# Kernel tuning notes

Hardware: AMD Instinct MI355X
Metric: run time of the kernel (lower is better)

## Reference

```python
import jax, jax.numpy as jnp
import numpy as np

B, V = 128, 128000
N_GREEDY = 8  # rows with temperature == 0 to exercise the argmax fallback


def setup_inputs() -> dict:
    key = jax.random.key(0)
    k1, k2, k3, k4 = jax.random.split(key, 4)
    logits = jax.random.normal(k1, (B, V), dtype=jnp.float32)
    temperatures = jax.random.uniform(k2, (B, 1), dtype=jnp.float32, minval=0.1, maxval=1.5)
    temperatures = temperatures.at[:N_GREEDY].set(0.0)  # greedy rows
    top_ps = 0.5 + 0.5 * jax.random.uniform(k3, (B, 1), dtype=jnp.float32)  # in [0.5, 1.0]
    top_ks = jax.random.randint(k4, (B, 1), 1, 64).astype(jnp.float32)  # stored as float, like torch code
    return {"logits": logits, "temperatures": temperatures, "top_ps": top_ps, "top_ks": top_ks}


def reference(logits, temperatures, top_ps, top_ks):
    # Temperature scale (temp==0 rows use safe temperature 1.0, overridden by greedy below)
    safe_t = jnp.where(temperatures == 0.0, 1.0, temperatures)  # [B,1]
    scaled = logits / safe_t  # [B,V] -- this is the `probs` returned by the torch module

    probs = jax.nn.softmax(scaled, axis=-1)  # [B,V]

    # Descending sort over vocab
    order = jnp.argsort(-probs, axis=-1)                      # [B,V] int
    sorted_probs = jnp.take_along_axis(probs, order, axis=-1)  # [B,V]
    cum = jnp.cumsum(sorted_probs, axis=-1)                    # [B,V]

    ranks = jnp.arange(V, dtype=jnp.float32)[None, :]          # [1,V]
    keep_k = ranks < top_ks                                    # top-k mask  [B,V]
    keep_p = (cum - sorted_probs) < top_ps                     # top-p mask (cumprob before token < p)
    keep = (keep_k & keep_p) | (ranks == 0.0)                  # always keep the top-1 token

    # Joint filter + Gumbel-max sampling (equivalent to renormalize-then-categorical)
    logp = jnp.where(keep, jnp.log(sorted_probs), -jnp.inf)    # [B,V]
    g = jax.random.gumbel(jax.random.key(42), (B, V), dtype=jnp.float32)
    sampled_sorted = jnp.argmax(logp + g, axis=-1)             # [B] index in sorted space
    sampled = jnp.take_along_axis(order, sampled_sorted[:, None], axis=-1)[:, 0]  # back to vocab ids

    # Greedy fallback for temperature == 0 rows (argmax of ORIGINAL logits)
    greedy = jnp.argmax(logits, axis=-1)
    ids = jnp.where(temperatures[:, 0] == 0.0, greedy, sampled).astype(jnp.int32)

    return ids, scaled
```

## Files before the change

### kernel.cpp

```cpp
#include <hip/hip_runtime.h>
#include <stdint.h>

#define NB 128
#define NV 128000
#define TOPC 63

#define JPB 25
#define CH 5120
#define CH4 1280
#define K1T 256
#define QPT 5
#define HB 8192
#define HBW (HB / 2)
#define CSLOT 104
#define SCCAP (JPB * CSLOT)
#define NHB 2048
#define SNCAP 256
#define NBLK1 (NB * JPB)

#define WS_CS_OFF   0
#define WS_CS_BYTES ((size_t)NBLK1 * CSLOT * 4)
#define WS_M_OFF    (WS_CS_BYTES)
#define WS_S_OFF    (WS_M_OFF + NBLK1 * 4)
#define WS_CNT_OFF  (WS_S_OFF + NBLK1 * 4)
#define WS_CTR_OFF  (WS_CNT_OFF + NBLK1 * 4)
#define WS_CI_OFF   (WS_CTR_OFF + NB * 4)
#define WS_NEED     (WS_CI_OFF + (size_t)NBLK1 * CSLOT * 2)

#define NT 1024
#define NV4 (NV / 4)
#define NBINS 16384
#define CCAP 2048

typedef float f4 __attribute__((ext_vector_type(4)));

__device__ __forceinline__ uint32_t rotl32(uint32_t v, uint32_t d) {
  return (v << d) | (v >> (32u - d));
}

__device__ __forceinline__ void threefry2x32(uint32_t k0, uint32_t k1,
                                             uint32_t x0, uint32_t x1,
                                             uint32_t& o0, uint32_t& o1) {
  uint32_t ks2 = k0 ^ k1 ^ 0x1BD11BDAu;
  x0 += k0; x1 += k1;
#define TF_ROUND(r) { x0 += x1; x1 = rotl32(x1, (r)); x1 ^= x0; }
  TF_ROUND(13) TF_ROUND(15) TF_ROUND(26) TF_ROUND(6)
  x0 += k1;  x1 += ks2 + 1u;
  TF_ROUND(17) TF_ROUND(29) TF_ROUND(16) TF_ROUND(24)
  x0 += ks2; x1 += k0 + 2u;
  TF_ROUND(13) TF_ROUND(15) TF_ROUND(26) TF_ROUND(6)
  x0 += k0;  x1 += k1 + 3u;
  TF_ROUND(17) TF_ROUND(29) TF_ROUND(16) TF_ROUND(24)
  x0 += k1;  x1 += ks2 + 4u;
  TF_ROUND(13) TF_ROUND(15) TF_ROUND(26) TF_ROUND(6)
  x0 += ks2; x1 += k0 + 5u;
#undef TF_ROUND
  o0 = x0; o1 = x1;
}

__device__ __forceinline__ uint32_t jax_random_bits_u32(uint64_t n) {
  uint32_t o0, o1;
  threefry2x32(0u, 42u, (uint32_t)(n >> 32), (uint32_t)n, o0, o1);
  return o0 ^ o1;
}

__device__ __forceinline__ float gumbel_from_bits(uint32_t bits) {
  const float tiny = 1.17549435e-38f;
  float f = __uint_as_float(0x3f800000u | (bits >> 9)) - 1.0f;
  float u = f * 1.0f + tiny;
  u = fmaxf(tiny, u);
  return -logf(-logf(u));
}

__device__ __forceinline__ uint32_t sortkey(float x) {
  uint32_t b = __float_as_uint(x);
  uint32_t mask = (uint32_t)((int32_t)b >> 31) | 0x80000000u;
  return b ^ mask;
}

__device__ __forceinline__ float div_exact(float a, float st, float ry) {
  float q0 = a * ry;
  float r  = __builtin_fmaf(-st, q0, a);
  return __builtin_fmaf(r, ry, q0);
}

__global__ __launch_bounds__(K1T) void k1_scan(
    const float* __restrict__ logits, const float* __restrict__ temps,
    float* __restrict__ out, uint32_t* __restrict__ cand_s,
    uint16_t* __restrict__ cand_i, float* __restrict__ m_arr,
    float* __restrict__ S_arr, uint32_t* __restrict__ cnt_arr) {

  __shared__ uint32_t histw[HBW];
  __shared__ uint32_t ssum[K1T];
  __shared__ float swm[4], sws[4];
  __shared__ uint32_t swc[4];
  __shared__ int s_tstar;
  __shared__ uint32_t s_cutkey, s_lcnt;

  const int bid = blockIdx.x;
  const int r = bid / JPB, j = bid - r * JPB;
  const int t = threadIdx.x;
  const int lane = t & 63, wv = t >> 6;
  const float temp = temps[r];
  const float st = (temp == 0.0f) ? 1.0f : temp;
  const float ry = 1.0f / st;

  const f4* __restrict__ lrow4 = (const f4*)(logits + (size_t)r * NV + (size_t)j * CH);
  f4* __restrict__ srow4 = (f4*)(out + NB + (size_t)r * NV + (size_t)j * CH);

  for (int i = t; i < HBW; i += K1T) histw[i] = 0u;
  if (t == 0) { s_tstar = K1T - 1; s_lcnt = 0u; }
  __syncthreads();

  f4 sreg[QPT];
  float mx0 = -INFINITY, mx1 = -INFINITY, mx2 = -INFINITY, mx3 = -INFINITY;
  float sm0 = 0.0f, sm1 = 0.0f, sm2 = 0.0f, sm3 = 0.0f;
  #pragma unroll
  for (int q = 0; q < QPT; ++q) {
    int i = q * K1T + t;
    f4 x = lrow4[i];
    f4 s;
    s.x = div_exact(x.x, st, ry);
    s.y = div_exact(x.y, st, ry);
    s.z = div_exact(x.z, st, ry);
    s.w = div_exact(x.w, st, ry);
    srow4[i] = s;
    sreg[q] = s;
    mx0 = fmaxf(mx0, s.x); mx1 = fmaxf(mx1, s.y);
    mx2 = fmaxf(mx2, s.z); mx3 = fmaxf(mx3, s.w);
    sm0 += __expf(s.x); sm1 += __expf(s.y);
    sm2 += __expf(s.z); sm3 += __expf(s.w);
  }
  float mx = fmaxf(fmaxf(mx0, mx1), fmaxf(mx2, mx3));
  float sum = (sm0 + sm1) + (sm2 + sm3);
  #pragma unroll
  for (int off = 32; off > 0; off >>= 1) {
    mx = fmaxf(mx, __shfl_xor(mx, off));
    sum += __shfl_xor(sum, off);
  }
  if (lane == 0) { swm[wv] = mx; sws[wv] = sum; }
  __syncthreads();
  const float mxb = fmaxf(fmaxf(swm[0], swm[1]), fmaxf(swm[2], swm[3]));
  if (t == 0) {
    m_arr[bid] = mxb;
    S_arr[bid] = sws[0] + sws[1] + sws[2] + sws[3];
  }
  const float thr = mxb - 3.0f * ry;

  uint32_t myc = 0;
  #pragma unroll
  for (int q = 0; q < QPT; ++q) {
    float sv[4] = {sreg[q].x, sreg[q].y, sreg[q].z, sreg[q].w};
    #pragma unroll
    for (int c = 0; c < 4; ++c) {
      if (sv[c] >= thr) {
        uint32_t b = sortkey(sv[c]) >> 19;
        atomicAdd(&histw[b >> 1], (b & 1) ? 65536u : 1u);
        ++myc;
      }
    }
  }
  #pragma unroll
  for (int off = 32; off > 0; off >>= 1) myc += __shfl_xor(myc, off);
  if (lane == 0) swc[wv] = myc;
  __syncthreads();
  const uint32_t tot = swc[0] + swc[1] + swc[2] + swc[3];
  if (tot < 63u) {
    for (int i = t; i < HBW; i += K1T) histw[i] = 0u;
    __syncthreads();
    #pragma unroll
    for (int q = 0; q < QPT; ++q) {
      float sv[4] = {sreg[q].x, sreg[q].y, sreg[q].z, sreg[q].w};
      #pragma unroll
      for (int c = 0; c < 4; ++c) {
        uint32_t b = sortkey(sv[c]) >> 19;
        atomicAdd(&histw[b >> 1], (b & 1) ? 65536u : 1u);
      }
    }
    __syncthreads();
  }

  uint32_t sloc = 0;
  #pragma unroll
  for (int u = 0; u < 16; ++u) {
    uint32_t w = histw[t * 16 + u];
    sloc += (w & 0xFFFFu) + (w >> 16);
  }
  ssum[t] = sloc;
  __syncthreads();
  for (int off = 1; off < K1T; off <<= 1) {
    uint32_t v = ssum[t] + ((t + off < K1T) ? ssum[t + off] : 0u);
    __syncthreads();
    ssum[t] = v;
    __syncthreads();
  }
  if (ssum[t] >= 63u && (t == K1T - 1 || ssum[t + 1] < 63u)) s_tstar = t;
  __syncthreads();
  if (t == 0) {
    int ts = s_tstar;
    uint32_t running = (ts == K1T - 1) ? 0u : ssum[ts + 1];
    int cutbin = ts * 32;
    for (int q = 31; q >= 0; --q) {
      uint32_t w = histw[ts * 16 + (q >> 1)];
      uint32_t c = (q & 1) ? (w >> 16) : (w & 0xFFFFu);
      running += c;
      if (running >= 63u) { cutbin = ts * 32 + q; break; }
    }
    s_cutkey = (uint32_t)cutbin << 19;
  }
  __syncthreads();
  const uint32_t cutkey = s_cutkey;

  uint32_t* __restrict__ mys = cand_s + (size_t)bid * CSLOT;
  uint16_t* __restrict__ myi = cand_i + (size_t)bid * CSLOT;
  #pragma unroll
  for (int q = 0; q < QPT; ++q) {
    float sv[4] = {sreg[q].x, sreg[q].y, sreg[q].z, sreg[q].w};
    #pragma unroll
    for (int c = 0; c < 4; ++c) {
      if (sortkey(sv[c]) >= cutkey) {
        uint32_t pos = atomicAdd(&s_lcnt, 1u);
        if (pos < CSLOT) {
          mys[pos] = __float_as_uint(sv[c]);
          myi[pos] = (uint16_t)((q * K1T + t) * 4 + c);
        }
      }
    }
  }
  __syncthreads();
  if (t == 0) cnt_arr[bid] = (s_lcnt < CSLOT) ? s_lcnt : (uint32_t)CSLOT;
}

__global__ __launch_bounds__(K1T) void k2_final(
    const float* __restrict__ temps, const float* __restrict__ topps,
    const float* __restrict__ topks, const uint32_t* __restrict__ cand_s,
    const uint16_t* __restrict__ cand_i, const float* __restrict__ m_arr,
    const float* __restrict__ S_arr, const uint32_t* __restrict__ cnt_arr,
    float* __restrict__ out) {

  __shared__ unsigned long long sc[SCCAP];
  __shared__ uint32_t nhist[NHB];
  __shared__ unsigned long long sn[SNCAP];
  __shared__ float sm8[32], ss8[32];
  __shared__ uint32_t scnt8[JPB];
  __shared__ uint32_t swsum[4];
  __shared__ uint32_t s_cutp, s_scnt;
  __shared__ uint32_t soff[JPB + 1];
  __shared__ float s_m, s_Z;
  __shared__ float sp[TOPC], scum[TOPC], slv[TOPC];
  __shared__ int sidx_[TOPC];

  const int r = blockIdx.x;
  const int t = threadIdx.x;
  const int lane = t & 63, wv = t >> 6;
  const float temp = temps[r];

  if (t < 32) {
    sm8[t] = (t < JPB) ? m_arr[r * JPB + t] : -INFINITY;
    ss8[t] = (t < JPB) ? S_arr[r * JPB + t] : 0.0f;
  }
  if (t < JPB) scnt8[t] = cnt_arr[r * JPB + t];
  for (int i = t; i < NHB; i += K1T) nhist[i] = 0u;
  __syncthreads();
  if (t == 0) {
    float m = -INFINITY;
    for (int q = 0; q < JPB; ++q) m = fmaxf(m, sm8[q]);
    float Sr = 0.0f;
    for (int q = 0; q < JPB; ++q) Sr += ss8[q];
    s_m = m;
    s_Z = Sr * expf(-m);
    uint32_t off = 0;
    for (int q = 0; q < JPB; ++q) { soff[q] = off; off += scnt8[q]; }
    soff[JPB] = off;
    s_scnt = 0u;
  }
  __syncthreads();
  const float m = s_m, Z = s_Z;
  const int total = (int)soff[JPB];

  for (int e = t; e < total; e += K1T) {
    int q = 0;
    while (e >= (int)soff[q + 1]) ++q;
    int slot = (r * JPB + q) * CSLOT + (e - (int)soff[q]);
    float s = __uint_as_float(cand_s[slot]);
    uint32_t idx = (uint32_t)q * CH + (uint32_t)cand_i[slot];
    float p = expf(s - m) / Z;
    unsigned long long v = ((unsigned long long)__float_as_uint(p) << 32)
                         | (unsigned long long)(0xFFFFFFFFu - idx);
    sc[e] = v;
    atomicAdd(&nhist[__float_as_uint(p) >> 21], 1u);
  }
  __syncthreads();

  uint32_t nloc = 0;
  #pragma unroll
  for (int u = 0; u < 8; ++u) nloc += nhist[t * 8 + u];
  uint32_t ns = nloc;
  #pragma unroll
  for (int off = 1; off < 64; off <<= 1) {
    uint32_t v = __shfl_down(ns, off);
    if (lane + off < 64) ns += v;
  }
  if (lane == 0) swsum[wv] = ns;
  __syncthreads();
  #pragma unroll
  for (int w2 = 0; w2 < 4; ++w2)
    if (w2 > wv) ns += swsum[w2];
  if (ns >= 63u && (ns - nloc) < 63u) {
    uint32_t running = ns - nloc;
    int cutbin = t * 8;
    for (int u = 7; u >= 0; --u) {
      running += nhist[t * 8 + u];
      if (running >= 63u) { cutbin = t * 8 + u; break; }
    }
    s_cutp = (uint32_t)cutbin << 21;
  }
  __syncthreads();
  const uint32_t cutp = s_cutp;

  for (int e = t; e < total; e += K1T) {
    unsigned long long v = sc[e];
    if ((uint32_t)(v >> 32) >= cutp) {
      uint32_t pos = atomicAdd(&s_scnt, 1u);
      if (pos < SNCAP) sn[pos] = v;
    }
  }
  __syncthreads();
  const uint32_t scnt = s_scnt;
  if (t < SNCAP && t >= (int)scnt) sn[t] = 0ull;
  __syncthreads();

  for (int k = 2; k <= SNCAP; k <<= 1) {
    for (int jj = k >> 1; jj > 0; jj >>= 1) {
      int e = t;
      int ixj = e ^ jj;
      if (ixj > e) {
        unsigned long long a = sn[e], c = sn[ixj];
        bool desc = ((e & k) == 0);
        if (desc ? (a < c) : (a > c)) { sn[e] = c; sn[ixj] = a; }
      }
      __syncthreads();
    }
  }

  if (t < TOPC) {
    unsigned long long kv = sn[t];
    sp[t] = __uint_as_float((uint32_t)(kv >> 32));
    sidx_[t] = (int)(0xFFFFFFFFu - (uint32_t)(kv & 0xFFFFFFFFull));
  }
  __syncthreads();
  if (t == 0) {
    float L0[63], L1[31], L2[15], L3[7], L4[3];
    for (int i = 0; i < 63; ++i) L0[i] = sp[i];
    for (int i = 0; i < 31; ++i) L1[i] = L0[2*i] + L0[2*i+1];
    for (int i = 0; i < 15; ++i) L2[i] = L1[2*i] + L1[2*i+1];
    for (int i = 0; i < 7;  ++i) L3[i] = L2[2*i] + L2[2*i+1];
    for (int i = 0; i < 3;  ++i) L4[i] = L3[2*i] + L3[2*i+1];
    float S5 = L4[0] + L4[1];
    float S4[3]; S4[0] = L4[0]; S4[1] = S5; S4[2] = S5 + L4[2];
    float S3[7]; S3[0] = L3[0];
    for (int k = 0; k < 3; ++k) { S3[2*k+1] = S4[k]; if (2*k+2 < 7)  S3[2*k+2] = S4[k] + L3[2*k+2]; }
    float S2[15]; S2[0] = L2[0];
    for (int k = 0; k < 7; ++k) { S2[2*k+1] = S3[k]; if (2*k+2 < 15) S2[2*k+2] = S3[k] + L2[2*k+2]; }
    float S1[31]; S1[0] = L1[0];
    for (int k = 0; k < 15; ++k){ S1[2*k+1] = S2[k]; if (2*k+2 < 31) S1[2*k+2] = S2[k] + L1[2*k+2]; }
    scum[0] = L0[0];
    for (int k = 0; k < 31; ++k){ scum[2*k+1] = S1[k]; if (2*k+2 < 63) scum[2*k+2] = S1[k] + L0[2*k+2]; }
  }
  __syncthreads();
  if (t < TOPC) {
    const float topp = topps[r];
    const float topk = topks[r];
    bool keep = (((float)t < topk) && ((scum[t] - sp[t]) < topp)) || (t == 0);
    uint32_t bits = jax_random_bits_u32((uint64_t)r * NV + (uint64_t)t);
    float g = gumbel_from_bits(bits);
    slv[t] = keep ? (logf(sp[t]) + g) : -INFINITY;
  }
  __syncthreads();
  if (t == 0) {
    float best = slv[0]; int br = 0;
    for (int q = 1; q < TOPC; ++q)
      if (slv[q] > best) { best = slv[q]; br = q; }
    int id = (temp == 0.0f) ? sidx_[0] : sidx_[br];
    out[r] = (float)id;
  }
}


__global__ __launch_bounds__(NT) void sampler_kernel(
    const float* __restrict__ logits, const float* __restrict__ temps,
    const float* __restrict__ topps, const float* __restrict__ topks,
    float* __restrict__ out) {

  __shared__ union {
    uint32_t hist[NBINS];
    unsigned long long cand[CCAP];
  } sh;
  __shared__ uint32_t ssum[NT];
  __shared__ float redf[NT];
  __shared__ uint32_t s_cutkey, s_cnt;
  __shared__ int s_tstar;
  __shared__ float sp[TOPC], scum[TOPC], slv[TOPC];
  __shared__ int sidx_[TOPC];

  const int b = blockIdx.x;
  const int t = threadIdx.x;
  const float temp = temps[b];
  const float st = (temp == 0.0f) ? 1.0f : temp;
  const float topp = topps[b];
  const float topk = topks[b];

  const float4* __restrict__ lrow = (const float4*)(logits + (size_t)b * NV);
  float4* __restrict__ srow = (float4*)(out + NB + (size_t)b * NV);

  for (int i = t; i < NBINS; i += NT) sh.hist[i] = 0u;
  if (t == 0) s_tstar = NT - 1;

  float lmax = -INFINITY;
  for (int i = t; i < NV4; i += NT) {
    float4 x = lrow[i];
    float4 s;
    s.x = x.x / st; s.y = x.y / st; s.z = x.z / st; s.w = x.w / st;
    srow[i] = s;
    lmax = fmaxf(lmax, fmaxf(fmaxf(s.x, s.y), fmaxf(s.z, s.w)));
  }
  redf[t] = lmax;
  __syncthreads();
  for (int off = NT / 2; off > 0; off >>= 1) {
    if (t < off) redf[t] = fmaxf(redf[t], redf[t + off]);
    __syncthreads();
  }
  const float m = redf[0];
  __syncthreads();

  float lsum = 0.0f;
  for (int i = t; i < NV4; i += NT) {
    float4 x = lrow[i];
    float s0 = x.x / st, s1 = x.y / st, s2 = x.z / st, s3 = x.w / st;
    lsum += expf(s0 - m); lsum += expf(s1 - m);
    lsum += expf(s2 - m); lsum += expf(s3 - m);
    atomicAdd(&sh.hist[sortkey(s0) >> 18], 1u);
    atomicAdd(&sh.hist[sortkey(s1) >> 18], 1u);
    atomicAdd(&sh.hist[sortkey(s2) >> 18], 1u);
    atomicAdd(&sh.hist[sortkey(s3) >> 18], 1u);
  }
  redf[t] = lsum;
  __syncthreads();
  for (int off = NT / 2; off > 0; off >>= 1) {
    if (t < off) redf[t] += redf[t + off];
    __syncthreads();
  }
  const float Z = redf[0];
  __syncthreads();

  uint32_t sloc = 0;
  #pragma unroll
  for (int j = 0; j < 16; ++j) sloc += sh.hist[t * 16 + j];
  ssum[t] = sloc;
  __syncthreads();
  for (int off = 1; off < NT; off <<= 1) {
    uint32_t v = ssum[t] + ((t + off < NT) ? ssum[t + off] : 0u);
    __syncthreads();
    ssum[t] = v;
    __syncthreads();
  }
  if (ssum[t] >= 63u && (t == NT - 1 || ssum[t + 1] < 63u)) s_tstar = t;
  __syncthreads();
  if (t == 0) {
    int ts = s_tstar;
    uint32_t running = (ts == NT - 1) ? 0u : ssum[ts + 1];
    int cutbin = ts * 16;
    for (int j = 15; j >= 0; --j) {
      running += sh.hist[ts * 16 + j];
      if (running >= 63u) { cutbin = ts * 16 + j; break; }
    }
    s_cutkey = (uint32_t)cutbin << 18;
    s_cnt = 0u;
  }
  __syncthreads();
  const uint32_t cutkey = s_cutkey;

  for (int i = t; i < NV4; i += NT) {
    float4 x = lrow[i];
    float sv[4];
    sv[0] = x.x / st; sv[1] = x.y / st; sv[2] = x.z / st; sv[3] = x.w / st;
    #pragma unroll
    for (int j = 0; j < 4; ++j) {
      uint32_t key = sortkey(sv[j]);
      if (key >= cutkey) {
        float p = expf(sv[j] - m) / Z;
        uint32_t pos = atomicAdd(&s_cnt, 1u);
        if (pos < CCAP) {
          uint32_t idx = (uint32_t)(i * 4 + j);
          sh.cand[pos] = ((unsigned long long)__float_as_uint(p) << 32)
                       | (unsigned long long)(0xFFFFFFFFu - idx);
        }
      }
    }
  }
  __syncthreads();
  const uint32_t cnt = s_cnt;
  for (int e = t; e < CCAP; e += NT)
    if ((uint32_t)e >= cnt) sh.cand[e] = 0ull;
  __syncthreads();

  for (uint32_t k = 2; k <= CCAP; k <<= 1) {
    for (uint32_t j = k >> 1; j > 0; j >>= 1) {
      for (int e = t; e < CCAP; e += NT) {
        uint32_t ixj = (uint32_t)e ^ j;
        if (ixj > (uint32_t)e) {
          unsigned long long a = sh.cand[e], c = sh.cand[ixj];
          bool desc = (((uint32_t)e & k) == 0u);
          if (desc ? (a < c) : (a > c)) { sh.cand[e] = c; sh.cand[ixj] = a; }
        }
      }
      __syncthreads();
    }
  }

  if (t < TOPC) {
    unsigned long long kv = sh.cand[t];
    sp[t] = __uint_as_float((uint32_t)(kv >> 32));
    sidx_[t] = (int)(0xFFFFFFFFu - (uint32_t)(kv & 0xFFFFFFFFull));
  }
  __syncthreads();
  if (t == 0) {
    float L0[63], L1[31], L2[15], L3[7], L4[3];
    for (int i = 0; i < 63; ++i) L0[i] = sp[i];
    for (int i = 0; i < 31; ++i) L1[i] = L0[2*i] + L0[2*i+1];
    for (int i = 0; i < 15; ++i) L2[i] = L1[2*i] + L1[2*i+1];
    for (int i = 0; i < 7;  ++i) L3[i] = L2[2*i] + L2[2*i+1];
    for (int i = 0; i < 3;  ++i) L4[i] = L3[2*i] + L3[2*i+1];
    float S5 = L4[0] + L4[1];
    float S4[3]; S4[0] = L4[0]; S4[1] = S5; S4[2] = S5 + L4[2];
    float S3[7]; S3[0] = L3[0];
    for (int k = 0; k < 3; ++k) { S3[2*k+1] = S4[k]; if (2*k+2 < 7)  S3[2*k+2] = S4[k] + L3[2*k+2]; }
    float S2[15]; S2[0] = L2[0];
    for (int k = 0; k < 7; ++k) { S2[2*k+1] = S3[k]; if (2*k+2 < 15) S2[2*k+2] = S3[k] + L2[2*k+2]; }
    float S1[31]; S1[0] = L1[0];
    for (int k = 0; k < 15; ++k){ S1[2*k+1] = S2[k]; if (2*k+2 < 31) S1[2*k+2] = S2[k] + L1[2*k+2]; }
    scum[0] = L0[0];
    for (int k = 0; k < 31; ++k){ scum[2*k+1] = S1[k]; if (2*k+2 < 63) scum[2*k+2] = S1[k] + L0[2*k+2]; }
  }
  __syncthreads();
  if (t < TOPC) {
    bool keep = (((float)t < topk) && ((scum[t] - sp[t]) < topp)) || (t == 0);
    uint32_t bits = jax_random_bits_u32((uint64_t)b * NV + (uint64_t)t);
    float g = gumbel_from_bits(bits);
    slv[t] = keep ? (logf(sp[t]) + g) : -INFINITY;
  }
  __syncthreads();
  if (t == 0) {
    float best = slv[0]; int br = 0;
    for (int q = 1; q < TOPC; ++q)
      if (slv[q] > best) { best = slv[q]; br = q; }
    int id = (temp == 0.0f) ? sidx_[0] : sidx_[br];
    out[b] = (float)id;
  }
}

extern "C" void kernel_launch(void* const* d_in, const int* in_sizes, int n_in,
                              void* d_out, int out_size, void* d_ws, size_t ws_size,
                              hipStream_t stream) {
  const float* logits = (const float*)d_in[0];
  const float* temps  = (const float*)d_in[1];
  const float* topps  = (const float*)d_in[2];
  const float* topks  = (const float*)d_in[3];
  float* out = (float*)d_out;

  if (ws_size >= WS_NEED) {
    uint32_t* cand_s  = (uint32_t*)((char*)d_ws + WS_CS_OFF);
    uint16_t* cand_i  = (uint16_t*)((char*)d_ws + WS_CI_OFF);
    float*    m_arr   = (float*)((char*)d_ws + WS_M_OFF);
    float*    S_arr   = (float*)((char*)d_ws + WS_S_OFF);
    uint32_t* cnt_arr = (uint32_t*)((char*)d_ws + WS_CNT_OFF);
    hipLaunchKernelGGL(k1_scan, dim3(NBLK1), dim3(K1T), 0, stream,
                       logits, temps, out, cand_s, cand_i, m_arr, S_arr, cnt_arr);
    hipLaunchKernelGGL(k2_final, dim3(NB), dim3(K1T), 0, stream,
                       temps, topps, topks, cand_s, cand_i,
                       m_arr, S_arr, cnt_arr, out);
  } else {
    hipLaunchKernelGGL(sampler_kernel, dim3(NB), dim3(NT), 0, stream,
                       logits, temps, topps, topks, out);
  }
}
```

Baseline: 51.76 us.

## Use max-relative linear histogram for candidate cutoff with radix fallback

In the scan kernel, a single 256-bin histogram over the scaled distance from the block max (a window of about 2.2 raw-logit units) replaces the thresholded radix-key histogram. A wave-shuffle prefix scan over those bins finds the cut, and candidates are written directly. The old 8192-bin radix path runs only when the count falls outside [63, CSLOT]. The final kernel drops the serial prefix-offset computation and iterates over fixed per-block slots, masking by count. This trades some wasted iterations over empty slots for less serial work.

```diff
diff --git a/kernel.cpp b/kernel.cpp
--- a/kernel.cpp
+++ b/kernel.cpp
@@ -12,6 +12,7 @@
 #define QPT 5
 #define HB 8192
 #define HBW (HB / 2)
+#define WINSD 2.2f
 #define CSLOT 104
 #define SCCAP (JPB * CSLOT)
 #define NHB 2048
@@ -93,9 +94,9 @@
   __shared__ uint32_t histw[HBW];
   __shared__ uint32_t ssum[K1T];
   __shared__ float swm[4], sws[4];
-  __shared__ uint32_t swc[4];
+  __shared__ uint32_t wtot[4];
   __shared__ int s_tstar;
-  __shared__ uint32_t s_cutkey, s_lcnt;
+  __shared__ uint32_t s_cutbin, s_cutkey, s_lcnt;
 
   const int bid = blockIdx.x;
   const int r = bid / JPB, j = bid - r * JPB;
@@ -108,9 +109,8 @@
   const f4* __restrict__ lrow4 = (const f4*)(logits + (size_t)r * NV + (size_t)j * CH);
   f4* __restrict__ srow4 = (f4*)(out + NB + (size_t)r * NV + (size_t)j * CH);
 
-  for (int i = t; i < HBW; i += K1T) histw[i] = 0u;
-  if (t == 0) { s_tstar = K1T - 1; s_lcnt = 0u; }
-  __syncthreads();
+  histw[t] = 0u;
+  if (t == 0) { s_lcnt = 0u; s_tstar = K1T - 1; s_cutbin = 255u; }
 
   f4 sreg[QPT];
   float mx0 = -INFINITY, mx1 = -INFINITY, mx2 = -INFINITY, mx3 = -INFINITY;
@@ -145,41 +145,76 @@
     m_arr[bid] = mxb;
     S_arr[bid] = sws[0] + sws[1] + sws[2] + sws[3];
   }
-  const float thr = mxb - 3.0f * ry;
-
-  uint32_t myc = 0;
+  const float F = (256.0f / WINSD) * st;
+
   #pragma unroll
   for (int q = 0; q < QPT; ++q) {
     float sv[4] = {sreg[q].x, sreg[q].y, sreg[q].z, sreg[q].w};
     #pragma unroll
     for (int c = 0; c < 4; ++c) {
-      if (sv[c] >= thr) {
-        uint32_t b = sortkey(sv[c]) >> 19;
-        atomicAdd(&histw[b >> 1], (b & 1) ? 65536u : 1u);
-        ++myc;
+      float d = (mxb - sv[c]) * F;
+      if (d < 256.0f) atomicAdd(&histw[(uint32_t)d], 1u);
+    }
+  }
+  __syncthreads();
+
+  {
+    uint32_t c = histw[t];
+    uint32_t ps = c;
+    #pragma unroll
+    for (int off = 1; off < 64; off <<= 1) {
+      uint32_t v = __shfl_up(ps, off);
+      if (lane >= off) ps += v;
+    }
+    if (lane == 63) wtot[wv] = ps;
+    __syncthreads();
+    uint32_t add = 0;
+    #pragma unroll
+    for (int w2 = 0; w2 < 4; ++w2)
+      if (w2 < wv) add += wtot[w2];
+    ps += add;
+    if (ps >= 63u && (ps - c) < 63u) s_cutbin = (uint32_t)t;
+  }
+  __syncthreads();
+  const uint32_t cutbin = s_cutbin;
+
+  uint32_t* __restrict__ mys = cand_s + (size_t)bid * CSLOT;
+  uint16_t* __restrict__ myi = cand_i + (size_t)bid * CSLOT;
+  #pragma unroll
+  for (int q = 0; q < QPT; ++q) {
+    float sv[4] = {sreg[q].x, sreg[q].y, sreg[q].z, sreg[q].w};
+    #pragma unroll
+    for (int c = 0; c < 4; ++c) {
+      float d = (mxb - sv[c]) * F;
+      if (d < 256.0f && (uint32_t)d <= cutbin) {
+        uint32_t pos = atomicAdd(&s_lcnt, 1u);
+        if (pos < CSLOT) {
+          mys[pos] = __float_as_uint(sv[c]);
+          myi[pos] = (uint16_t)((q * K1T + t) * 4 + c);
+        }
       }
     }
   }
-  #pragma unroll
-  for (int off = 32; off > 0; off >>= 1) myc += __shfl_xor(myc, off);
-  if (lane == 0) swc[wv] = myc;
-  __syncthreads();
-  const uint32_t tot = swc[0] + swc[1] + swc[2] + swc[3];
-  if (tot < 63u) {
-    for (int i = t; i < HBW; i += K1T) histw[i] = 0u;
-    __syncthreads();
+  __syncthreads();
+  const uint32_t lc = s_lcnt;
+  if (lc >= 63u && lc <= (uint32_t)CSLOT) {
+    if (t == 0) cnt_arr[bid] = lc;
+    return;
+  }
+
+  if (t == 0) s_lcnt = 0u;
+  for (int i = t; i < HBW; i += K1T) histw[i] = 0u;
+  __syncthreads();
+  #pragma unroll
+  for (int q = 0; q < QPT; ++q) {
+    float sv[4] = {sreg[q].x, sreg[q].y, sreg[q].z, sreg[q].w};
     #pragma unroll
-    for (int q = 0; q < QPT; ++q) {
-      float sv[4] = {sreg[q].x, sreg[q].y, sreg[q].z, sreg[q].w};
-      #pragma unroll
-      for (int c = 0; c < 4; ++c) {
-        uint32_t b = sortkey(sv[c]) >> 19;
-        atomicAdd(&histw[b >> 1], (b & 1) ? 65536u : 1u);
-      }
-    }
-    __syncthreads();
-  }
-
+    for (int c = 0; c < 4; ++c) {
+      uint32_t b = sortkey(sv[c]) >> 19;
+      atomicAdd(&histw[b >> 1], (b & 1) ? 65536u : 1u);
+    }
+  }
+  __syncthreads();
   uint32_t sloc = 0;
   #pragma unroll
   for (int u = 0; u < 16; ++u) {
@@ -199,20 +234,17 @@
   if (t == 0) {
     int ts = s_tstar;
     uint32_t running = (ts == K1T - 1) ? 0u : ssum[ts + 1];
-    int cutbin = ts * 32;
+    int cb = ts * 32;
     for (int q = 31; q >= 0; --q) {
       uint32_t w = histw[ts * 16 + (q >> 1)];
       uint32_t c = (q & 1) ? (w >> 16) : (w & 0xFFFFu);
       running += c;
-      if (running >= 63u) { cutbin = ts * 32 + q; break; }
-    }
-    s_cutkey = (uint32_t)cutbin << 19;
+      if (running >= 63u) { cb = ts * 32 + q; break; }
+    }
+    s_cutkey = (uint32_t)cb << 19;
   }
   __syncthreads();
   const uint32_t cutkey = s_cutkey;
-
-  uint32_t* __restrict__ mys = cand_s + (size_t)bid * CSLOT;
-  uint16_t* __restrict__ myi = cand_i + (size_t)bid * CSLOT;
   #pragma unroll
   for (int q = 0; q < QPT; ++q) {
     float sv[4] = {sreg[q].x, sreg[q].y, sreg[q].z, sreg[q].w};
@@ -245,7 +277,6 @@
   __shared__ uint32_t scnt8[JPB];
   __shared__ uint32_t swsum[4];
   __shared__ uint32_t s_cutp, s_scnt;
-  __shared__ uint32_t soff[JPB + 1];
   __shared__ float s_m, s_Z;
   __shared__ float sp[TOPC], scum[TOPC], slv[TOPC];
   __shared__ int sidx_[TOPC];
@@ -269,26 +300,23 @@
     for (int q = 0; q < JPB; ++q) Sr += ss8[q];
     s_m = m;
     s_Z = Sr * expf(-m);
-    uint32_t off = 0;
-    for (int q = 0; q < JPB; ++q) { soff[q] = off; off += scnt8[q]; }
-    soff[JPB] = off;
     s_scnt = 0u;
   }
   __syncthreads();
   const float m = s_m, Z = s_Z;
-  const int total = (int)soff[JPB];
-
-  for (int e = t; e < total; e += K1T) {
-    int q = 0;
-    while (e >= (int)soff[q + 1]) ++q;
-    int slot = (r * JPB + q) * CSLOT + (e - (int)soff[q]);
-    float s = __uint_as_float(cand_s[slot]);
-    uint32_t idx = (uint32_t)q * CH + (uint32_t)cand_i[slot];
-    float p = expf(s - m) / Z;
-    unsigned long long v = ((unsigned long long)__float_as_uint(p) << 32)
-                         | (unsigned long long)(0xFFFFFFFFu - idx);
-    sc[e] = v;
-    atomicAdd(&nhist[__float_as_uint(p) >> 21], 1u);
+
+  for (int e = t; e < SCCAP; e += K1T) {
+    int q = e / CSLOT;
+    int slot = e - q * CSLOT;
+    if (slot < (int)scnt8[q]) {
+      int gs = (r * JPB + q) * CSLOT + slot;
+      float s = __uint_as_float(cand_s[gs]);
+      uint32_t idx = (uint32_t)q * CH + (uint32_t)cand_i[gs];
+      float p = expf(s - m) / Z;
+      sc[e] = ((unsigned long long)__float_as_uint(p) << 32)
+            | (unsigned long long)(0xFFFFFFFFu - idx);
+      atomicAdd(&nhist[__float_as_uint(p) >> 21], 1u);
+    }
   }
   __syncthreads();
 
@@ -318,11 +346,15 @@
   __syncthreads();
   const uint32_t cutp = s_cutp;
 
-  for (int e = t; e < total; e += K1T) {
-    unsigned long long v = sc[e];
-    if ((uint32_t)(v >> 32) >= cutp) {
-      uint32_t pos = atomicAdd(&s_scnt, 1u);
-      if (pos < SNCAP) sn[pos] = v;
+  for (int e = t; e < SCCAP; e += K1T) {
+    int q = e / CSLOT;
+    int slot = e - q * CSLOT;
+    if (slot < (int)scnt8[q]) {
+      unsigned long long v = sc[e];
+      if ((uint32_t)(v >> 32) >= cutp) {
+        uint32_t pos = atomicAdd(&s_scnt, 1u);
+        if (pos < SNCAP) sn[pos] = v;
+      }
     }
   }
   __syncthreads();
```

Result: faster. 49.14 us (-5.1%).
